# Kernel optimization log

Measured on AMD Instinct MI355X. Metric: run time of the kernel, lower is better.

## Reference

```python
import jax, jax.numpy as jnp
import numpy as np

NODE_DIM = 128
N_NODES = 100000
N_REL = 32
N_EDGES = 500000
MLP_DIM = 64  # mlp_edge_model_dim
TEMPERATURE = 0.5
BIAS = 0.0 + 0.0001


def _xavier(key, shape):
    fan_in, fan_out = shape[1], shape[0]
    limit = float(np.sqrt(6.0 / (fan_in + fan_out)))
    return jax.random.uniform(key, shape, jnp.float32, -limit, limit)


def setup_inputs() -> dict:
    key = jax.random.key(0)
    k1, k2, k3, k4, k5, k6, k7 = jax.random.split(key, 7)
    edge_index = jax.random.randint(k1, (2, N_EDGES), 0, N_NODES, dtype=jnp.int64)
    edge_type = jax.random.randint(k2, (N_EDGES,), 0, N_REL, dtype=jnp.int64)
    all_embed = jax.random.normal(k3, (N_NODES, NODE_DIM), jnp.float32)
    relation_emb = jax.random.normal(k4, (N_REL, NODE_DIM), jnp.float32)
    u = jax.random.uniform(k5, (N_EDGES,), jnp.float32)  # stand-in for torch.rand
    # MLP params: Linear(3*node_dim -> 3*mlp_dim), ReLU, Linear(3*mlp_dim -> 1)
    W1 = _xavier(k6, (3 * MLP_DIM, 3 * NODE_DIM))
    b1 = jnp.zeros((3 * MLP_DIM,), jnp.float32)
    W2 = _xavier(k7, (1, 3 * MLP_DIM))
    b2 = jnp.zeros((1,), jnp.float32)
    return {"edge_index": edge_index, "edge_type": edge_type,
            "all_embed": all_embed, "relation_emb": relation_emb, "u": u,
            "W1": W1, "b1": b1, "W2": W2, "b2": b2}


def reference(edge_index, edge_type, all_embed, relation_emb, u, W1, b1, W2, b2):
    head_emb = all_embed[edge_index[0, :]]          # [E, d]
    tail_emb = all_embed[edge_index[1, :]]          # [E, d]
    latent_emb = relation_emb[edge_type]            # [E, d]
    x = jnp.concatenate([head_emb, tail_emb, latent_emb], axis=1)  # [E, 3d]
    h = jax.nn.relu(x @ W1.T + b1)                  # [E, 3*mlp_dim]
    weight = (h @ W2.T + b2)[:, 0]                  # [E]
    # eps = (bias - (1-bias)) * u + (1-bias), eps in [bias, 1-bias]
    eps = (2.0 * BIAS - 1.0) * u + (1.0 - BIAS)
    gate_inputs = jnp.log(eps) - jnp.log1p(-eps)
    gate_inputs = (gate_inputs + weight) / TEMPERATURE
    aug_edge_weight = jax.nn.sigmoid(gate_inputs)   # [E]
    return aug_edge_weight
```

## Files before the change

kernel.cpp:

```cpp
#include <hip/hip_runtime.h>
#include <hip/hip_bf16.h>

#define N_NODES     100000
#define NODE_DIM    128
#define N_REL       32
#define N_EDGES_C   500000
#define H_DIM       192
#define P_COLS      384
#define TILE_ROWS   64
#define NTILES      1563
#define NBLK        256

typedef __bf16 bf16x8 __attribute__((ext_vector_type(8)));
typedef float  f32x4  __attribute__((ext_vector_type(4)));
typedef unsigned int u32;

__device__ __forceinline__ ushort f2b(float x) {
    __hip_bfloat16 h = __float2bfloat16(x);
    return *reinterpret_cast<ushort*>(&h);
}

__device__ __forceinline__ void unpack2(unsigned v, float& lo, float& hi) {
    union { unsigned u; float f; } a, b;
    a.u = v << 16;
    b.u = v & 0xffff0000u;
    lo = a.f; hi = b.f;
}

__device__ __forceinline__ void gload_lds16(const void* g, void* l) {
    __builtin_amdgcn_global_load_lds(
        (const __attribute__((address_space(1))) u32*)g,
        (__attribute__((address_space(3))) u32*)l, 16, 0, 0);
}

__global__ __launch_bounds__(256) void build_b_kernel(
        const float* __restrict__ W1, ushort* __restrict__ Bmat) {
    int idx = blockIdx.x * 256 + threadIdx.x;
    if (idx >= P_COLS * NODE_DIM) return;
    int c = idx >> 7, k = idx & 127;
    float v = (c < H_DIM) ? W1[(size_t)c * P_COLS + k]
                          : W1[(size_t)(c - H_DIM) * P_COLS + NODE_DIM + k];
    Bmat[idx] = f2b(v);
}

__global__ void rel_precompute_kernel(const float* __restrict__ rel,
                                      const float* __restrict__ W1,
                                      const float* __restrict__ b1,
                                      float* __restrict__ Rb) {
    int r = blockIdx.x;
    int j = threadIdx.x;
    const float* re = rel + r * NODE_DIM;
    const float* w  = W1 + (size_t)j * P_COLS + 2 * NODE_DIM;
    float acc = b1[j];
    #pragma unroll 8
    for (int k = 0; k < NODE_DIM; ++k)
        acc = fmaf(re[k], w[k], acc);
    Rb[r * H_DIM + j] = acc;
}

__global__ __launch_bounds__(512) void node_mfma_kernel(
        const float* __restrict__ embF,
        const ushort* __restrict__ Bmat,
        ushort* __restrict__ Pb) {
    __shared__ float ldsA[2][TILE_ROWS * NODE_DIM];

    const int tid  = threadIdx.x;
    const int wid  = tid >> 6;
    const int lane = tid & 63;
    const int r16  = lane & 15;
    const int kgrp = lane >> 4;
    const int wr   = wid & 1;
    const int wc   = wid >> 1;
    const int colw = wc * 96;

    bf16x8 Bf[6][4];
    {
        const ushort* Bbase = Bmat + (size_t)(colw + r16) * NODE_DIM + kgrp * 8;
        #pragma unroll
        for (int ct = 0; ct < 6; ++ct)
            #pragma unroll
            for (int ks = 0; ks < 4; ++ks)
                Bf[ct][ks] = *(const bf16x8*)(Bbase + (size_t)ct * 16 * NODE_DIM + ks * 32);
    }

    const size_t A_CLAMP = (size_t)N_NODES * NODE_DIM * sizeof(float) - 16;

    auto stage = [&](int p, int tile) {
        const size_t tbase = (size_t)tile * (TILE_ROWS * NODE_DIM * 4);
        #pragma unroll
        for (int i = 0; i < 4; ++i) {
            const int L    = i * 8192 + tid * 16;
            const int rowl = L >> 9;
            const int g    = (L >> 5) & 15;
            const int h16  = L & 16;
            size_t src = tbase +
                (size_t)((rowl << 9) | ((g ^ (rowl & 15)) << 5) | h16);
            if (src > A_CLAMP) src = A_CLAMP;
            gload_lds16((const char*)embF + src, (char*)&ldsA[p][0] + L);
        }
    };

    int tile = blockIdx.x;
    stage(0, tile);
    int p = 0;

    for (; tile < NTILES; tile += NBLK) {
        __syncthreads();

        if (tile + NBLK < NTILES)
            stage(p ^ 1, tile + NBLK);

        bf16x8 a[2][4];
        #pragma unroll
        for (int rt = 0; rt < 2; ++rt) {
            const int rowl  = wr * 32 + rt * 16 + r16;
            const int rbase = rowl * NODE_DIM;
            const int sw    = rowl & 15;
            #pragma unroll
            for (int ks = 0; ks < 4; ++ks) {
                const int gl = (kgrp + ks * 4) ^ sw;
                const float* pf = &ldsA[p][rbase + gl * 8];
                float4 v0 = *(const float4*)pf;
                float4 v1 = *(const float4*)(pf + 4);
                bf16x8 r;
                r[0] = (__bf16)v0.x; r[1] = (__bf16)v0.y;
                r[2] = (__bf16)v0.z; r[3] = (__bf16)v0.w;
                r[4] = (__bf16)v1.x; r[5] = (__bf16)v1.y;
                r[6] = (__bf16)v1.z; r[7] = (__bf16)v1.w;
                a[rt][ks] = r;
            }
        }

        f32x4 acc[2][6] = {};
        #pragma unroll
        for (int ks = 0; ks < 4; ++ks)
            #pragma unroll
            for (int ct = 0; ct < 6; ++ct) {
                acc[0][ct] = __builtin_amdgcn_mfma_f32_16x16x32_bf16(Bf[ct][ks], a[0][ks], acc[0][ct], 0, 0, 0);
                acc[1][ct] = __builtin_amdgcn_mfma_f32_16x16x32_bf16(Bf[ct][ks], a[1][ks], acc[1][ct], 0, 0, 0);
            }

        const int rowbase = tile * TILE_ROWS + wr * 32;
        #pragma unroll
        for (int rt = 0; rt < 2; ++rt) {
            const int prow = rowbase + rt * 16 + r16;
            if (prow < N_NODES) {
                ushort* rowp = Pb + (size_t)prow * P_COLS + colw + kgrp * 4;
                #pragma unroll
                for (int ct = 0; ct < 6; ++ct) {
                    unsigned lo = (unsigned)f2b(acc[rt][ct][0]) |
                                  ((unsigned)f2b(acc[rt][ct][1]) << 16);
                    unsigned hi = (unsigned)f2b(acc[rt][ct][2]) |
                                  ((unsigned)f2b(acc[rt][ct][3]) << 16);
                    uint2 v; v.x = lo; v.y = hi;
                    *(uint2*)(rowp + ct * 16) = v;
                }
            }
        }

        p ^= 1;
    }
}

__global__ __launch_bounds__(256) void edge_kernel(
        const int* __restrict__ edge_index,
        const int* __restrict__ edge_type,
        const ushort* __restrict__ Pb,
        const float* __restrict__ Rb,
        const float* __restrict__ u,
        const float* __restrict__ W2,
        const float* __restrict__ b2,
        float* __restrict__ out) {
    const int tid  = threadIdx.x;
    const int wave = tid >> 6;
    const int lane = tid & 63;
    const int g    = lane >> 3;
    const int sub  = lane & 7;

    const int e = blockIdx.x * 32 + wave * 8 + g;

    const int head = edge_index[e];
    const int tail = edge_index[N_EDGES_C + e];
    const int rel  = edge_type[e];

    const ushort* Ph = Pb + (size_t)head * P_COLS;
    const ushort* Pt = Pb + (size_t)tail * P_COLS + H_DIM;
    const int j0 = sub * 8;

    uint4 h0 = *(const uint4*)(Ph + j0);
    uint4 h1 = *(const uint4*)(Ph + j0 + 64);
    uint4 h2 = *(const uint4*)(Ph + j0 + 128);
    uint4 t0 = *(const uint4*)(Pt + j0);
    uint4 t1 = *(const uint4*)(Pt + j0 + 64);
    uint4 t2 = *(const uint4*)(Pt + j0 + 128);

    const float* Rr = Rb + rel * H_DIM + j0;
    const float* Wp = W2 + j0;

    float acc = 0.f;
    #pragma unroll
    for (int c = 0; c < 3; ++c) {
        uint4 hv = (c == 0) ? h0 : (c == 1) ? h1 : h2;
        uint4 tv = (c == 0) ? t0 : (c == 1) ? t1 : t2;
        float4 r0 = *(const float4*)(Rr + c * 64);
        float4 r1 = *(const float4*)(Rr + c * 64 + 4);
        float4 w0 = *(const float4*)(Wp + c * 64);
        float4 w1 = *(const float4*)(Wp + c * 64 + 4);

        float h0f,h1f,h2f,h3f,h4f,h5f,h6f,h7f;
        float t0f,t1f,t2f,t3f,t4f,t5f,t6f,t7f;
        unpack2(hv.x, h0f, h1f); unpack2(hv.y, h2f, h3f);
        unpack2(hv.z, h4f, h5f); unpack2(hv.w, h6f, h7f);
        unpack2(tv.x, t0f, t1f); unpack2(tv.y, t2f, t3f);
        unpack2(tv.z, t4f, t5f); unpack2(tv.w, t6f, t7f);

        float s;
        s = fmaxf(h0f + t0f + r0.x, 0.f); acc = fmaf(s, w0.x, acc);
        s = fmaxf(h1f + t1f + r0.y, 0.f); acc = fmaf(s, w0.y, acc);
        s = fmaxf(h2f + t2f + r0.z, 0.f); acc = fmaf(s, w0.z, acc);
        s = fmaxf(h3f + t3f + r0.w, 0.f); acc = fmaf(s, w0.w, acc);
        s = fmaxf(h4f + t4f + r1.x, 0.f); acc = fmaf(s, w1.x, acc);
        s = fmaxf(h5f + t5f + r1.y, 0.f); acc = fmaf(s, w1.y, acc);
        s = fmaxf(h6f + t6f + r1.z, 0.f); acc = fmaf(s, w1.z, acc);
        s = fmaxf(h7f + t7f + r1.w, 0.f); acc = fmaf(s, w1.w, acc);
    }

    acc += __shfl_xor(acc, 1);
    acc += __shfl_xor(acc, 2);
    acc += __shfl_xor(acc, 4);

    if (sub == 0) {
        float weight = acc + b2[0];
        float uu  = u[e];
        float eps = fmaf(-0.9998f, uu, 0.9999f);
        float gi  = (logf(eps) - log1pf(-eps) + weight) * 2.0f;
        out[e] = 1.f / (1.f + expf(-gi));
    }
}

extern "C" void kernel_launch(void* const* d_in, const int* in_sizes, int n_in,
                              void* d_out, int out_size, void* d_ws, size_t ws_size,
                              hipStream_t stream) {
    const int*   edge_index   = (const int*)d_in[0];
    const int*   edge_type    = (const int*)d_in[1];
    const float* all_embed    = (const float*)d_in[2];
    const float* relation_emb = (const float*)d_in[3];
    const float* u            = (const float*)d_in[4];
    const float* W1           = (const float*)d_in[5];
    const float* b1           = (const float*)d_in[6];
    const float* W2           = (const float*)d_in[7];
    const float* b2           = (const float*)d_in[8];
    float*       out          = (float*)d_out;

    char* ws = (char*)d_ws;
    ushort* Bmat = (ushort*)ws;
    ws += (size_t)P_COLS * NODE_DIM * sizeof(ushort);
    float*  Rb   = (float*)ws;
    ws += (size_t)N_REL * H_DIM * sizeof(float);
    ushort* Pb   = (ushort*)ws;

    build_b_kernel<<<(P_COLS * NODE_DIM + 255) / 256, 256, 0, stream>>>(W1, Bmat);
    rel_precompute_kernel<<<N_REL, H_DIM, 0, stream>>>(relation_emb, W1, b1, Rb);

    node_mfma_kernel<<<NBLK, 512, 0, stream>>>(all_embed, Bmat, Pb);

    edge_kernel<<<N_EDGES_C / 32, 256, 0, stream>>>(
        edge_index, edge_type, Pb, Rb, u, W2, b2, out);
}
```

Baseline: 116.9 us.

## Triple-buffer node GEMM staging with vmcnt waits and packed-float edge math

Changes the node MFMA kernel from 64-row tiles with 512 threads to 32-row tiles with 256 threads on 512 blocks. It also replaces double buffering with a three-stage LDS ring that waits on vmcnt instead of a full sync, and uses a new 16-byte XOR swizzle. The edge kernel switches to two-wide float vectors so the compiler can emit packed FP32 add, max and multiply. The goal is more overlap of the embedding loads with the MFMA work and fewer VALU instructions per edge, at the cost of hand-tuned vmcnt counts that have to match the number of issued loads.

New measurement: 102.2 us. -12.5%, faster.

```diff
diff --git a/kernel.cpp b/kernel.cpp
--- a/kernel.cpp
+++ b/kernel.cpp
@@ -7,24 +7,18 @@
 #define N_EDGES_C   500000
 #define H_DIM       192
 #define P_COLS      384
-#define TILE_ROWS   64
-#define NTILES      1563
-#define NBLK        256
+#define TILE_ROWS   32
+#define NTILES      3125
+#define NBLK        512
 
 typedef __bf16 bf16x8 __attribute__((ext_vector_type(8)));
 typedef float  f32x4  __attribute__((ext_vector_type(4)));
+typedef float  f32x2  __attribute__((ext_vector_type(2)));
 typedef unsigned int u32;
 
 __device__ __forceinline__ ushort f2b(float x) {
     __hip_bfloat16 h = __float2bfloat16(x);
     return *reinterpret_cast<ushort*>(&h);
-}
-
-__device__ __forceinline__ void unpack2(unsigned v, float& lo, float& hi) {
-    union { unsigned u; float f; } a, b;
-    a.u = v << 16;
-    b.u = v & 0xffff0000u;
-    lo = a.f; hi = b.f;
 }
 
 __device__ __forceinline__ void gload_lds16(const void* g, void* l) {
@@ -58,20 +52,18 @@
     Rb[r * H_DIM + j] = acc;
 }
 
-__global__ __launch_bounds__(512) void node_mfma_kernel(
+__global__ __launch_bounds__(256) void node_mfma_kernel(
         const float* __restrict__ embF,
         const ushort* __restrict__ Bmat,
         ushort* __restrict__ Pb) {
-    __shared__ float ldsA[2][TILE_ROWS * NODE_DIM];
+    __shared__ float ldsA[3][TILE_ROWS * NODE_DIM];
 
     const int tid  = threadIdx.x;
     const int wid  = tid >> 6;
     const int lane = tid & 63;
     const int r16  = lane & 15;
     const int kgrp = lane >> 4;
-    const int wr   = wid & 1;
-    const int wc   = wid >> 1;
-    const int colw = wc * 96;
+    const int colw = wid * 96;
 
     bf16x8 Bf[6][4];
     {
@@ -89,12 +81,12 @@
         const size_t tbase = (size_t)tile * (TILE_ROWS * NODE_DIM * 4);
         #pragma unroll
         for (int i = 0; i < 4; ++i) {
-            const int L    = i * 8192 + tid * 16;
-            const int rowl = L >> 9;
-            const int g    = (L >> 5) & 15;
-            const int h16  = L & 16;
+            const int L    = i * 4096 + tid * 16;
+            const int u16  = L >> 4;
+            const int rowl = u16 >> 5;
+            const int g16  = u16 & 31;
             size_t src = tbase +
-                (size_t)((rowl << 9) | ((g ^ (rowl & 15)) << 5) | h16);
+                (size_t)((rowl << 9) | ((g16 ^ rowl) << 4));
             if (src > A_CLAMP) src = A_CLAMP;
             gload_lds16((const char*)embF + src, (char*)&ldsA[p][0] + L);
         }
@@ -102,26 +94,30 @@
 
     int tile = blockIdx.x;
     stage(0, tile);
+    if (tile + NBLK < NTILES) stage(1, tile + NBLK);
     int p = 0;
 
     for (; tile < NTILES; tile += NBLK) {
-        __syncthreads();
-
-        if (tile + NBLK < NTILES)
-            stage(p ^ 1, tile + NBLK);
+        const bool more1 = (tile + NBLK)     < NTILES;
+        const bool more2 = (tile + 2 * NBLK) < NTILES;
+
+        if (more1) asm volatile("s_waitcnt vmcnt(4)" ::: "memory");
+        else       asm volatile("s_waitcnt vmcnt(0)" ::: "memory");
+        __builtin_amdgcn_s_barrier();
+
+        if (more2) stage((p + 2) % 3, tile + 2 * NBLK);
 
         bf16x8 a[2][4];
         #pragma unroll
         for (int rt = 0; rt < 2; ++rt) {
-            const int rowl  = wr * 32 + rt * 16 + r16;
-            const int rbase = rowl * NODE_DIM;
-            const int sw    = rowl & 15;
+            const int rowl = rt * 16 + r16;
             #pragma unroll
             for (int ks = 0; ks < 4; ++ks) {
-                const int gl = (kgrp + ks * 4) ^ sw;
-                const float* pf = &ldsA[p][rbase + gl * 8];
-                float4 v0 = *(const float4*)pf;
-                float4 v1 = *(const float4*)(pf + 4);
+                const int gbase = 2 * (kgrp + ks * 4);
+                const float* pa = &ldsA[p][rowl * NODE_DIM + ((gbase    ) ^ rowl) * 4];
+                const float* pb = &ldsA[p][rowl * NODE_DIM + ((gbase + 1) ^ rowl) * 4];
+                float4 v0 = *(const float4*)pa;
+                float4 v1 = *(const float4*)pb;
                 bf16x8 r;
                 r[0] = (__bf16)v0.x; r[1] = (__bf16)v0.y;
                 r[2] = (__bf16)v0.z; r[3] = (__bf16)v0.w;
@@ -140,7 +136,7 @@
                 acc[1][ct] = __builtin_amdgcn_mfma_f32_16x16x32_bf16(Bf[ct][ks], a[1][ks], acc[1][ct], 0, 0, 0);
             }
 
-        const int rowbase = tile * TILE_ROWS + wr * 32;
+        const int rowbase = tile * TILE_ROWS;
         #pragma unroll
         for (int rt = 0; rt < 2; ++rt) {
             const int prow = rowbase + rt * 16 + r16;
@@ -158,8 +154,22 @@
             }
         }
 
-        p ^= 1;
-    }
+        p = (p + 1) % 3;
+    }
+}
+
+__device__ __forceinline__ void pairproc(unsigned h, unsigned t,
+                                         f32x2 r, f32x2 w, f32x2& acc) {
+    union { unsigned u[2]; f32x2 f; } A, B;
+    A.u[0] = h << 16;          A.u[1] = h & 0xffff0000u;
+    B.u[0] = t << 16;          B.u[1] = t & 0xffff0000u;
+    f32x2 s = A.f + B.f + r;
+#if __has_builtin(__builtin_elementwise_max)
+    s = __builtin_elementwise_max(s, (f32x2)(0.f));
+#else
+    s[0] = fmaxf(s[0], 0.f); s[1] = fmaxf(s[1], 0.f);
+#endif
+    acc += s * w;
 }
 
 __global__ __launch_bounds__(256) void edge_kernel(
@@ -197,34 +207,23 @@
     const float* Rr = Rb + rel * H_DIM + j0;
     const float* Wp = W2 + j0;
 
-    float acc = 0.f;
+    f32x2 acc2 = {0.f, 0.f};
     #pragma unroll
     for (int c = 0; c < 3; ++c) {
         uint4 hv = (c == 0) ? h0 : (c == 1) ? h1 : h2;
         uint4 tv = (c == 0) ? t0 : (c == 1) ? t1 : t2;
-        float4 r0 = *(const float4*)(Rr + c * 64);
-        float4 r1 = *(const float4*)(Rr + c * 64 + 4);
-        float4 w0 = *(const float4*)(Wp + c * 64);
-        float4 w1 = *(const float4*)(Wp + c * 64 + 4);
-
-        float h0f,h1f,h2f,h3f,h4f,h5f,h6f,h7f;
-        float t0f,t1f,t2f,t3f,t4f,t5f,t6f,t7f;
-        unpack2(hv.x, h0f, h1f); unpack2(hv.y, h2f, h3f);
-        unpack2(hv.z, h4f, h5f); unpack2(hv.w, h6f, h7f);
-        unpack2(tv.x, t0f, t1f); unpack2(tv.y, t2f, t3f);
-        unpack2(tv.z, t4f, t5f); unpack2(tv.w, t6f, t7f);
-
-        float s;
-        s = fmaxf(h0f + t0f + r0.x, 0.f); acc = fmaf(s, w0.x, acc);
-        s = fmaxf(h1f + t1f + r0.y, 0.f); acc = fmaf(s, w0.y, acc);
-        s = fmaxf(h2f + t2f + r0.z, 0.f); acc = fmaf(s, w0.z, acc);
-        s = fmaxf(h3f + t3f + r0.w, 0.f); acc = fmaf(s, w0.w, acc);
-        s = fmaxf(h4f + t4f + r1.x, 0.f); acc = fmaf(s, w1.x, acc);
-        s = fmaxf(h5f + t5f + r1.y, 0.f); acc = fmaf(s, w1.y, acc);
-        s = fmaxf(h6f + t6f + r1.z, 0.f); acc = fmaf(s, w1.z, acc);
-        s = fmaxf(h7f + t7f + r1.w, 0.f); acc = fmaf(s, w1.w, acc);
-    }
-
+        f32x4 r4a = *(const f32x4*)(Rr + c * 64);
+        f32x4 r4b = *(const f32x4*)(Rr + c * 64 + 4);
+        f32x4 w4a = *(const f32x4*)(Wp + c * 64);
+        f32x4 w4b = *(const f32x4*)(Wp + c * 64 + 4);
+
+        pairproc(hv.x, tv.x, r4a.xy, w4a.xy, acc2);
+        pairproc(hv.y, tv.y, r4a.zw, w4a.zw, acc2);
+        pairproc(hv.z, tv.z, r4b.xy, w4b.xy, acc2);
+        pairproc(hv.w, tv.w, r4b.zw, w4b.zw, acc2);
+    }
+
+    float acc = acc2[0] + acc2[1];
     acc += __shfl_xor(acc, 1);
     acc += __shfl_xor(acc, 2);
     acc += __shfl_xor(acc, 4);
@@ -262,7 +261,7 @@
     build_b_kernel<<<(P_COLS * NODE_DIM + 255) / 256, 256, 0, stream>>>(W1, Bmat);
     rel_precompute_kernel<<<N_REL, H_DIM, 0, stream>>>(relation_emb, W1, b1, Rb);
 
-    node_mfma_kernel<<<NBLK, 512, 0, stream>>>(all_embed, Bmat, Pb);
+    node_mfma_kernel<<<NBLK, 256, 0, stream>>>(all_embed, Bmat, Pb);
 
     edge_kernel<<<N_EDGES_C / 32, 256, 0, stream>>>(
         edge_index, edge_type, Pb, Rb, u, W2, b2, out);
```
